# Kernel tuning notes

Hardware: AMD Instinct MI355X
Metric: run time of the kernel (lower is better)

Reference implementation:

```python
import jax, jax.numpy as jnp
import numpy as np
import math

HEADS = 16
HIDDEN = 1024
HEAD_DIM = HIDDEN // HEADS


def _split_heads(t):
    # (B, S, H*D) -> (B, H, S, D)
    b, s, _ = t.shape
    return t.reshape(b, s, HEADS, HEAD_DIM).transpose(0, 2, 1, 3)


def _rel_shift(x):
    # Transformer-XL relative shift: pad a zero column, reshape, drop first row.
    b, h, q, L = x.shape
    zero_pad = jnp.zeros((b, h, q, 1), dtype=x.dtype)
    x_padded = jnp.concatenate([zero_pad, x], axis=-1).reshape(b, h, L + 1, q)
    return x_padded[:, :, 1:, :].reshape(b, h, q, L)


def setup_inputs() -> dict:
    key = jax.random.key(0)
    ks = jax.random.split(key, 12)
    B, S, MEM = 4, 1024, 1024
    KV = S + MEM
    inp = {
        "x": jax.random.normal(ks[0], (B, S, HIDDEN), jnp.float32),
        "u": jax.random.normal(ks[1], (HEADS, HEAD_DIM), jnp.float32),
        "v_rel": jax.random.normal(ks[2], (HEADS, HEAD_DIM), jnp.float32),
        "rel": jax.random.normal(ks[3], (1, KV, HIDDEN), jnp.float32),
        "mask": jnp.zeros((1, 1, S, KV), jnp.int32),
        "past_key_values": jax.random.normal(ks[4], (B, MEM, HIDDEN), jnp.float32),
        "Wq": jax.random.normal(ks[5], (HIDDEN, HIDDEN), jnp.float32) * 0.02,
        "Wk": jax.random.normal(ks[6], (HIDDEN, HIDDEN), jnp.float32) * 0.02,
        "Wv": jax.random.normal(ks[7], (HIDDEN, HIDDEN), jnp.float32) * 0.02,
        "Wr": jax.random.normal(ks[8], (HIDDEN, HIDDEN), jnp.float32) * 0.02,
        "Wfc": jax.random.normal(ks[9], (HIDDEN, HIDDEN), jnp.float32) * 0.02,
        "bfc": jnp.zeros((HIDDEN,), jnp.float32),
    }
    return inp


def reference(x, u, v_rel, rel, mask, past_key_values, Wq, Wk, Wv, Wr, Wfc, bfc):
    # Transformer-XL style relative-position multi-head attention (eval mode, dropout off).
    x_extra = jnp.concatenate([past_key_values, x], axis=1)  # (B, KV, H*D)
    q = _split_heads(x @ Wq.T)          # (B, H, S, D)
    k = _split_heads(x_extra @ Wk.T)    # (B, H, KV, D)
    v = _split_heads(x_extra @ Wv.T)    # (B, H, KV, D)
    # rel: (1, KV, HIDDEN) -> r: (1, H, KV, D)
    r = (rel @ Wr.T).reshape(1, rel.shape[1], HEADS, HEAD_DIM).transpose(0, 2, 1, 3)

    term_AC = jnp.einsum("bhsd,bhkd->bhsk", q + u[None, :, None, :], k)
    term_BD = jnp.einsum("bhsd,xhkd->bhsk", q + v_rel[None, :, None, :], r)
    term_BD = _rel_shift(term_BD)

    attn = (term_AC + term_BD) / math.sqrt(HEAD_DIM)
    attn = jnp.where(mask == 1, -jnp.inf, attn)
    attn = jax.nn.softmax(attn, axis=-1)
    attn = jnp.where(jnp.isnan(attn), 0.0, attn)  # nan-cleanup from fully-masked rows

    out = jnp.einsum("bhsk,bhkd->bhsd", attn, v)
    out = out.transpose(0, 2, 1, 3).reshape(x.shape[0], x.shape[1], HIDDEN)
    out = out @ Wfc.T + bfc + x
    return out
```

## Files before the change

kernel.cpp:

```cpp
#include <hip/hip_runtime.h>
#include <stdint.h>


typedef unsigned short u16;
typedef __bf16 v8bf __attribute__((ext_vector_type(8)));
typedef float v4f __attribute__((ext_vector_type(4)));
typedef short v4s __attribute__((ext_vector_type(4)));

__device__ __forceinline__ v4f mfma16(v8bf a, v8bf b, v4f c) {
  return __builtin_amdgcn_mfma_f32_16x16x32_bf16(a, b, c, 0, 0, 0);
}

__device__ __forceinline__ u16 f2bf(float f) {
  uint32_t u = __builtin_bit_cast(uint32_t, f);
  return (u16)((u + 0x7fffu + ((u >> 16) & 1u)) >> 16);
}

__device__ __forceinline__ void async16(const u16* g, u16* l) {
  __builtin_amdgcn_global_load_lds(
      (const __attribute__((address_space(1))) void*)g,
      (__attribute__((address_space(3))) void*)l, 16, 0, 0);
}

__device__ __forceinline__ float bperm(int idx, float v) {
  return __builtin_bit_cast(
      float, __builtin_amdgcn_ds_bpermute(idx, __builtin_bit_cast(int, v)));
}

#if defined(__has_builtin)
#if __has_builtin(__builtin_amdgcn_ds_read_tr16_b64)
#define HAS_TR16 1
#endif
#endif

__device__ __forceinline__ v8bf vfrag(const u16* p) {
  v4s lo, hi;
#ifdef HAS_TR16
  lo = __builtin_amdgcn_ds_read_tr16_b64(
      (__attribute__((address_space(3))) v4s*)p);
  hi = __builtin_amdgcn_ds_read_tr16_b64(
      (__attribute__((address_space(3))) v4s*)(p + 256));
#else
#pragma unroll
  for (int j = 0; j < 4; ++j) {
    lo[j] = (short)p[j * 16];
    hi[j] = (short)p[256 + j * 16];
  }
#endif
  return __builtin_bit_cast(v8bf,
                            __builtin_shufflevector(lo, hi, 0, 1, 2, 3, 4, 5, 6, 7));
}

__global__ void conv_all_k(const float* __restrict__ past, const float* __restrict__ x,
                           const float* __restrict__ rel, const float* __restrict__ Wq,
                           const float* __restrict__ Wk, const float* __restrict__ Wv,
                           const float* __restrict__ Wr, const float* __restrict__ Wfc,
                           u16* __restrict__ xe, u16* __restrict__ xb,
                           u16* __restrict__ relb, u16* __restrict__ wdst,
                           u16* __restrict__ zrow) {
  int bid = blockIdx.x;
  if (bid < 8192) {
    int idx = bid * 256 + threadIdx.x;
    int e = idx << 2;
    int row = e >> 10, col = e & 1023;
    int b = row >> 11, t = row & 2047;
    const float* src = (t < 1024) ? past + ((((size_t)(b << 10)) + t) << 10) + col
                                  : x + ((((size_t)(b << 10)) + (t - 1024)) << 10) + col;
    float4 v = *(const float4*)src;
    ushort4 o = make_ushort4(f2bf(v.x), f2bf(v.y), f2bf(v.z), f2bf(v.w));
    *(ushort4*)(xe + e) = o;
    if (t >= 1024) {
      size_t xbi = ((((size_t)(b << 10)) + (t - 1024)) << 10) + col;
      *(ushort4*)(xb + xbi) = o;
    }
  } else if (bid < 10240) {
    int e = ((bid - 8192) * 256 + threadIdx.x) << 2;
    float4 v = *(const float4*)(rel + e);
    *(ushort4*)(relb + e) =
        make_ushort4(f2bf(v.x), f2bf(v.y), f2bf(v.z), f2bf(v.w));
  } else if (bid < 15360) {
    int wb = bid - 10240;
    int wsel = wb >> 10;
    const float* src = (wsel == 0) ? Wq
                     : (wsel == 1) ? Wk
                     : (wsel == 2) ? Wv
                     : (wsel == 3) ? Wr : Wfc;
    int e = ((wb & 1023) * 256 + threadIdx.x) << 2;
    float4 v = *(const float4*)(src + e);
    *(ushort4*)(wdst + (((size_t)wsel) << 20) + e) =
        make_ushort4(f2bf(v.x), f2bf(v.y), f2bf(v.z), f2bf(v.w));
  } else {
    *(ushort4*)(zrow + threadIdx.x * 4) = make_ushort4(0, 0, 0, 0);
  }
}

__device__ __forceinline__ void gemm_body(const u16* A, const u16* Bw, u16* o0, u16* o1,
                                          bool dual, const float* bias0, const float* bias1,
                                          int row0, int col0, u16* lA, u16* lB) {
  int t = threadIdx.x;
  int w = t >> 6, lane = t & 63, q = lane >> 4, l = lane & 15;
  int wy = w >> 1, wx = w & 1;
  v4f acc[4][4];
#pragma unroll
  for (int i = 0; i < 4; i++)
#pragma unroll
    for (int j = 0; j < 4; j++) acc[i][j] = v4f{0.f, 0.f, 0.f, 0.f};

  for (int kb = 0; kb < 1024; kb += 32) {
    __syncthreads();
#pragma unroll
    for (int p = 0; p < 2; ++p) {
      int g = (p << 8) + (w << 6) + lane;
      int m = g >> 2, cp = g & 3;
      int c = cp ^ ((m >> 1) & 3);
      async16(A + (((size_t)(row0 + m)) << 10) + kb + (c << 3),
              lA + ((p << 8) + (w << 6)) * 8);
      async16(Bw + (((size_t)(col0 + m)) << 10) + kb + (c << 3),
              lB + ((p << 8) + (w << 6)) * 8);
    }
    __syncthreads();
    v8bf af[4], bfr[4];
#pragma unroll
    for (int mt = 0; mt < 4; ++mt) {
      int ml = (wy << 6) + (mt << 4) + l;
      af[mt] = *(const v8bf*)&lA[(ml << 5) + ((q ^ ((ml >> 1) & 3)) << 3)];
      int nl = (wx << 6) + (mt << 4) + l;
      bfr[mt] = *(const v8bf*)&lB[(nl << 5) + ((q ^ ((nl >> 1) & 3)) << 3)];
    }
#pragma unroll
    for (int mt = 0; mt < 4; ++mt)
#pragma unroll
      for (int nt = 0; nt < 4; ++nt)
        acc[mt][nt] = mfma16(af[mt], bfr[nt], acc[mt][nt]);
  }

  float b0[4], b1[4];
  if (dual) {
#pragma unroll
    for (int nt = 0; nt < 4; ++nt) {
      int gcol = col0 + (wx << 6) + (nt << 4) + l;
      b0[nt] = bias0[gcol];
      b1[nt] = bias1[gcol];
    }
  }
#pragma unroll
  for (int mt = 0; mt < 4; ++mt)
#pragma unroll
    for (int nt = 0; nt < 4; ++nt)
#pragma unroll
      for (int rr = 0; rr < 4; ++rr) {
        int grow = row0 + (wy << 6) + (mt << 4) + (q << 2) + rr;
        int gcol = col0 + (wx << 6) + (nt << 4) + l;
        size_t idx = (((size_t)grow) << 10) + gcol;
        float v = acc[mt][nt][rr];
        if (dual) {
          o0[idx] = f2bf(v + b0[nt]);
          o1[idx] = f2bf(v + b1[nt]);
        } else {
          o0[idx] = f2bf(v);
        }
      }
}

__launch_bounds__(256)
__global__ void gemm_qkvr(const u16* __restrict__ xb, const u16* __restrict__ xe,
                          const u16* __restrict__ relb, const u16* __restrict__ wqb,
                          const u16* __restrict__ wkb, const u16* __restrict__ wvb,
                          const u16* __restrict__ wrb, u16* __restrict__ Qu,
                          u16* __restrict__ Qv, u16* __restrict__ Kbf,
                          u16* __restrict__ Vbf, u16* __restrict__ Rpb,
                          const float* __restrict__ u, const float* __restrict__ vr) {
  __shared__ __align__(16) u16 lA[128 * 32];
  __shared__ __align__(16) u16 lB[128 * 32];
  int y = blockIdx.y;
  const u16 *A, *Bw;
  u16 *o0, *o1 = nullptr;
  bool dual = false;
  int row0;
  if (y < 32) {
    A = xb; Bw = wqb; o0 = Qu; o1 = Qv; dual = true; row0 = y << 7;
  } else if (y < 96) {
    A = xe; Bw = wkb; o0 = Kbf; row0 = (y - 32) << 7;
  } else if (y < 160) {
    A = xe; Bw = wvb; o0 = Vbf; row0 = (y - 96) << 7;
  } else {
    A = relb; Bw = wrb; o0 = Rpb; row0 = (y - 160) << 7;
  }
  gemm_body(A, Bw, o0, o1, dual, u, vr, row0, blockIdx.x << 7, lA, lB);
}

__launch_bounds__(256)
__global__ void gemm_fin(const u16* __restrict__ A, const u16* __restrict__ Bw,
                         float* __restrict__ of, const float* __restrict__ bias0,
                         const float* __restrict__ resid) {
  __shared__ __align__(16) u16 lA[128 * 32];
  __shared__ __align__(16) u16 lB[128 * 32];
  int t = threadIdx.x;
  int w = t >> 6, lane = t & 63, q = lane >> 4, l = lane & 15;
  int wy = w >> 1, wx = w & 1;
  int row0 = blockIdx.y << 7, col0 = blockIdx.x << 7;
  v4f acc[4][4];
#pragma unroll
  for (int i = 0; i < 4; i++)
#pragma unroll
    for (int j = 0; j < 4; j++) acc[i][j] = v4f{0.f, 0.f, 0.f, 0.f};

  for (int kb = 0; kb < 1024; kb += 32) {
    __syncthreads();
#pragma unroll
    for (int p = 0; p < 2; ++p) {
      int g = (p << 8) + (w << 6) + lane;
      int m = g >> 2, cp = g & 3;
      int c = cp ^ ((m >> 1) & 3);
      async16(A + (((size_t)(row0 + m)) << 10) + kb + (c << 3),
              lA + ((p << 8) + (w << 6)) * 8);
      async16(Bw + (((size_t)(col0 + m)) << 10) + kb + (c << 3),
              lB + ((p << 8) + (w << 6)) * 8);
    }
    __syncthreads();
    v8bf af[4], bfr[4];
#pragma unroll
    for (int mt = 0; mt < 4; ++mt) {
      int ml = (wy << 6) + (mt << 4) + l;
      af[mt] = *(const v8bf*)&lA[(ml << 5) + ((q ^ ((ml >> 1) & 3)) << 3)];
      int nl = (wx << 6) + (mt << 4) + l;
      bfr[mt] = *(const v8bf*)&lB[(nl << 5) + ((q ^ ((nl >> 1) & 3)) << 3)];
    }
#pragma unroll
    for (int mt = 0; mt < 4; ++mt)
#pragma unroll
      for (int nt = 0; nt < 4; ++nt)
        acc[mt][nt] = mfma16(af[mt], bfr[nt], acc[mt][nt]);
  }

  float b0[4];
#pragma unroll
  for (int nt = 0; nt < 4; ++nt) b0[nt] = bias0[col0 + (wx << 6) + (nt << 4) + l];
#pragma unroll
  for (int mt = 0; mt < 4; ++mt)
#pragma unroll
    for (int nt = 0; nt < 4; ++nt)
#pragma unroll
      for (int rr = 0; rr < 4; ++rr) {
        int grow = row0 + (wy << 6) + (mt << 4) + (q << 2) + rr;
        int gcol = col0 + (wx << 6) + (nt << 4) + l;
        size_t idx = (((size_t)grow) << 10) + gcol;
        of[idx] = acc[mt][nt][rr] + b0[nt] + resid[idx];
      }
}

__launch_bounds__(256, 3)
__global__ void attn_k(const u16* __restrict__ Qu, const u16* __restrict__ Qv,
                       const u16* __restrict__ Kb, const u16* __restrict__ Vb,
                       const u16* __restrict__ Rp, u16* __restrict__ AO) {
  __shared__ __align__(16) u16 lK[64 * 64];
  __shared__ __align__(16) u16 lV[8 * 528];
  __shared__ __align__(16) u16 lR[192 * 64];
  __shared__ __align__(16) u16 lP[4][16 * 72];

  int t = threadIdx.x;
  int w = t >> 6, lane = t & 63, q = lane >> 4, l = lane & 15;
  int i0 = blockIdx.x << 6;
  int bh = blockIdx.y, b = bh >> 4, h = bh & 15;

  v8bf fqu[2], fqv[2], fqv1[2];
  {
    int m = i0 + (w << 4) + l;
    const u16* pu = Qu + ((((size_t)(b << 10)) + m) << 10) + (h << 6);
    fqu[0] = *(const v8bf*)(pu + q * 8);
    fqu[1] = *(const v8bf*)(pu + 32 + q * 8);
    const u16* pv = Qv + ((((size_t)(b << 10)) + m) << 10) + (h << 6);
    fqv[0] = *(const v8bf*)(pv + q * 8);
    fqv[1] = *(const v8bf*)(pv + 32 + q * 8);
    int m1 = min(m + 1, 1023);
    const u16* pv1 = Qv + ((((size_t)(b << 10)) + m1) << 10) + (h << 6);
    fqv1[0] = *(const v8bf*)(pv1 + q * 8);
    fqv1[1] = *(const v8bf*)(pv1 + 32 + q * 8);
  }

  v4f accO[4];
#pragma unroll
  for (int i = 0; i < 4; i++) accO[i] = v4f{0.f, 0.f, 0.f, 0.f};
  float psum[4] = {0.f, 0.f, 0.f, 0.f};
  const float SC = 0.125f * 1.44269504088896340736f;

  u16* Pw = &lP[w][0];
  const u16* vtb = lV + q * 528 + l;
  int rbase = 48 - (w << 4);

  int gidx[4];
  bool ghi[4];
#pragma unroll
  for (int rr = 0; rr < 4; ++rr) {
    int s = l + 15 - ((q << 2) + rr);
    gidx[rr] = ((q << 4) + (s & 15)) << 2;
    ghi[rr] = (s & 16) != 0;
  }

  int rb0 = 960 - i0;
  int r192 = rb0 % 192;

#pragma unroll
  for (int p = 0; p < 4; ++p) {
    int off = (p << 5) + (w << 3);
    int base = r192 + off;
    if (base >= 192) base -= 192;
    int rr = off + (lane >> 3);
    int c = (lane & 7) ^ (rr & 7);
    async16(Rp + (((size_t)(rb0 + rr)) << 10) + (h << 6) + (c << 3),
            lR + (base << 6));
  }

  for (int jt = 0; jt < 32; ++jt) {
    int j0 = jt << 6;

    __syncthreads();
#pragma unroll
    for (int p = 0; p < 2; ++p) {
      int g = (p << 8) + t;
      int kv = g >> 3, cp = g & 7, c = cp ^ (kv & 7);
      async16(Kb + ((((size_t)(b << 11)) + j0 + kv) << 10) + (h << 6) + (c << 3),
              lK + ((p << 8) + (w << 6)) * 8);
    }
#pragma unroll
    for (int p = 0; p < 2; ++p) {
      int s = (p << 8) + t;
      int kv = ((s >> 5) << 2) + ((s >> 1) & 3);
      int d = (((s >> 3) & 3) << 4) + ((s & 1) << 3);
      async16(Vb + ((((size_t)(b << 11)) + j0 + kv) << 10) + (h << 6) + d,
              lV + ((p << 2) + w) * 528);
    }
    if (jt < 31) {
      int sb = r192 + 128;
      if (sb >= 192) sb -= 192;
#pragma unroll
      for (int p = 0; p < 2; ++p) {
        int off = (p << 5) + (w << 3);
        int rr = off + (lane >> 3);
        int c = (lane & 7) ^ (rr & 7);
        int rowg = rb0 + 128 + rr;
        if (rowg >= 2049) rowg -= 2049;
        async16(Rp + (((size_t)rowg) << 10) + (h << 6) + (c << 3),
                lR + ((sb + off) << 6));
      }
    }
    __syncthreads();

    __builtin_amdgcn_s_setprio(1);
    v4f sc[4];
#pragma unroll
    for (int nt = 0; nt < 4; ++nt) {
      v4f a = v4f{0.f, 0.f, 0.f, 0.f};
      int row = (nt << 4) + l;
      a = mfma16(fqu[0], *(const v8bf*)&lK[((row << 3) + (q ^ (row & 7))) << 3], a);
      a = mfma16(fqu[1], *(const v8bf*)&lK[((row << 3) + ((4 + q) ^ (row & 7))) << 3], a);
      sc[nt] = a;
    }

    v4f eacc[5];
#pragma unroll
    for (int et = 0; et < 5; ++et) {
      int ps = r192 + rbase + (et << 4);
      if (ps >= 192) ps -= 192;
      int rrow = ps + l;
      v8bf r0 = *(const v8bf*)&lR[((rrow << 3) + (q ^ (rrow & 7))) << 3];
      v8bf r1 = *(const v8bf*)&lR[((rrow << 3) + ((4 + q) ^ (rrow & 7))) << 3];
      v4f a = v4f{0.f, 0.f, 0.f, 0.f};
      if (__builtin_amdgcn_readfirstlane(rb0 + rbase + (et << 4)) >= 2048) {
        a = mfma16(fqv1[0], r0, a);
        a = mfma16(fqv1[1], r1, a);
      } else {
        a = mfma16(fqv[0], r0, a);
        a = mfma16(fqv[1], r1, a);
      }
      eacc[et] = a;
    }
    __builtin_amdgcn_s_setprio(0);

#pragma unroll
    for (int rr = 0; rr < 4; ++rr) {
      float r0 = bperm(gidx[rr], eacc[0][rr]);
      float r1 = bperm(gidx[rr], eacc[1][rr]);
      float r2 = bperm(gidx[rr], eacc[2][rr]);
      float r3 = bperm(gidx[rr], eacc[3][rr]);
      float r4 = bperm(gidx[rr], eacc[4][rr]);
      sc[0][rr] += ghi[rr] ? r1 : r0;
      sc[1][rr] += ghi[rr] ? r2 : r1;
      sc[2][rr] += ghi[rr] ? r3 : r2;
      sc[3][rr] += ghi[rr] ? r4 : r3;
    }

#pragma unroll
    for (int nt = 0; nt < 4; ++nt)
#pragma unroll
      for (int rr = 0; rr < 4; ++rr) {
        float pv = __builtin_amdgcn_exp2f(sc[nt][rr] * SC);
        psum[rr] += pv;
        Pw[((q << 2) + rr) * 72 + (nt << 4) + l] = __builtin_bit_cast(u16, (__bf16)pv);
      }

    v8bf fp0 = *(const v8bf*)&Pw[l * 72 + (q << 3)];
    v8bf fp1 = *(const v8bf*)&Pw[l * 72 + 32 + (q << 3)];
    __builtin_amdgcn_s_setprio(1);
#pragma unroll
    for (int nt = 0; nt < 4; ++nt) {
      accO[nt] = mfma16(fp0, vfrag(vtb + (nt << 6)), accO[nt]);
      accO[nt] = mfma16(fp1, vfrag(vtb + (nt << 6) + 2112), accO[nt]);
    }
    __builtin_amdgcn_s_setprio(0);

    rb0 += 64;
    r192 += 64;
    if (r192 >= 192) r192 -= 192;
  }

#pragma unroll
  for (int rr = 0; rr < 4; ++rr) {
    float v = psum[rr];
    v += __shfl_xor(v, 1);
    v += __shfl_xor(v, 2);
    v += __shfl_xor(v, 4);
    v += __shfl_xor(v, 8);
    psum[rr] = 1.0f / v;
  }
#pragma unroll
  for (int nt = 0; nt < 4; ++nt)
#pragma unroll
    for (int rr = 0; rr < 4; ++rr) {
      int i = i0 + (w << 4) + (q << 2) + rr;
      int col = (h << 6) + (nt << 4) + l;
      AO[((((size_t)(b << 10)) + i) << 10) + col] = f2bf(accO[nt][rr] * psum[rr]);
    }
}


extern "C" void kernel_launch(void* const* d_in, const int* in_sizes, int n_in,
                              void* d_out, int out_size, void* d_ws, size_t ws_size,
                              hipStream_t stream) {
  const float* x    = (const float*)d_in[0];
  const float* u    = (const float*)d_in[1];
  const float* vr   = (const float*)d_in[2];
  const float* rel  = (const float*)d_in[3];
  const float* past = (const float*)d_in[5];
  const float* Wq   = (const float*)d_in[6];
  const float* Wk   = (const float*)d_in[7];
  const float* Wv   = (const float*)d_in[8];
  const float* Wr   = (const float*)d_in[9];
  const float* Wfc  = (const float*)d_in[10];
  const float* bfc  = (const float*)d_in[11];
  float* out = (float*)d_out;

  char* ws = (char*)d_ws;
  u16* xe   = (u16*)(ws + 0);
  u16* xb   = (u16*)(ws + 16777216);
  u16* relb = (u16*)(ws + 25165824);
  u16* wqb  = (u16*)(ws + 29360128);
  u16* wkb  = (u16*)(ws + 31457280);
  u16* wvb  = (u16*)(ws + 33554432);
  u16* wrb  = (u16*)(ws + 35651584);
  u16* wfcb = (u16*)(ws + 37748736);
  u16* Qu   = (u16*)(ws + 39845888);
  u16* Qv   = (u16*)(ws + 48234496);
  u16* Kbf  = (u16*)(ws + 56623104);
  u16* Vbf  = (u16*)(ws + 73400320);
  u16* Rpb  = (u16*)(ws + 90177536);
  u16* AOb  = (u16*)(ws + 94373888);
  if (ws_size < 102762496ull) return;

  conv_all_k<<<dim3(15361), dim3(256), 0, stream>>>(
      past, x, rel, Wq, Wk, Wv, Wr, Wfc, xe, xb, relb, wqb, Rpb + 2048 * 1024);

  gemm_qkvr<<<dim3(8, 176), dim3(256), 0, stream>>>(
      xb, xe, relb, wqb, wkb, wvb, wrb, Qu, Qv, Kbf, Vbf, Rpb, u, vr);

  attn_k<<<dim3(16, 64), dim3(256), 0, stream>>>(Qu, Qv, Kbf, Vbf, Rpb, AOb);

  gemm_fin<<<dim3(8, 32), dim3(256), 0, stream>>>(AOb, wfcb, out, bfc, x);
}
```

Before: 386.2 us.

## Double attention query tile to 128 rows with 8 waves sharing K/V/R tiles

Each attention block now covers 128 query rows with 512 threads (8 waves), so each K, V and R tile loaded into LDS is reused by twice as many waves and global traffic per query row halves. The R ring buffer grows to 256 rows with power-of-two masking in place of the modulo-192 bookkeeping. The trailing __syncthreads is replaced by explicit vmcnt waits plus s_barrier. The grid shrinks to 512 blocks, which reduces parallelism, and the larger LDS footprint may limit occupancy.

```diff
diff --git a/kernel.cpp b/kernel.cpp
--- a/kernel.cpp
+++ b/kernel.cpp
@@ -249,18 +249,18 @@
       }
 }
 
-__launch_bounds__(256, 3)
+__launch_bounds__(512, 4)
 __global__ void attn_k(const u16* __restrict__ Qu, const u16* __restrict__ Qv,
                        const u16* __restrict__ Kb, const u16* __restrict__ Vb,
                        const u16* __restrict__ Rp, u16* __restrict__ AO) {
   __shared__ __align__(16) u16 lK[64 * 64];
   __shared__ __align__(16) u16 lV[8 * 528];
-  __shared__ __align__(16) u16 lR[192 * 64];
-  __shared__ __align__(16) u16 lP[4][16 * 72];
+  __shared__ __align__(16) u16 lR[256 * 64];
+  __shared__ __align__(16) u16 lP[8][16 * 72];
 
   int t = threadIdx.x;
   int w = t >> 6, lane = t & 63, q = lane >> 4, l = lane & 15;
-  int i0 = blockIdx.x << 6;
+  int i0 = blockIdx.x << 7;
   int bh = blockIdx.y, b = bh >> 4, h = bh & 15;
 
   v8bf fqu[2], fqv[2], fqv1[2];
@@ -286,7 +286,7 @@
 
   u16* Pw = &lP[w][0];
   const u16* vtb = lV + q * 528 + l;
-  int rbase = 48 - (w << 4);
+  int rbase = 112 - (w << 4);
 
   int gidx[4];
   bool ghi[4];
@@ -297,54 +297,48 @@
     ghi[rr] = (s & 16) != 0;
   }
 
-  int rb0 = 960 - i0;
-  int r192 = rb0 % 192;
-
-#pragma unroll
-  for (int p = 0; p < 4; ++p) {
-    int off = (p << 5) + (w << 3);
-    int base = r192 + off;
-    if (base >= 192) base -= 192;
-    int rr = off + (lane >> 3);
+  int rb0 = 896 - i0;
+
+#pragma unroll
+  for (int p = 0; p < 3; ++p) {
+    int rr = (p << 6) + (t >> 3);
     int c = (lane & 7) ^ (rr & 7);
+    int sb = ((rb0 + (p << 6)) & 255) + (w << 3);
     async16(Rp + (((size_t)(rb0 + rr)) << 10) + (h << 6) + (c << 3),
-            lR + (base << 6));
+            lR + (sb << 6));
   }
 
   for (int jt = 0; jt < 32; ++jt) {
     int j0 = jt << 6;
 
     __syncthreads();
-#pragma unroll
-    for (int p = 0; p < 2; ++p) {
-      int g = (p << 8) + t;
-      int kv = g >> 3, cp = g & 7, c = cp ^ (kv & 7);
+
+    {
+      int kv = t >> 3, cp = t & 7, c = cp ^ (kv & 7);
       async16(Kb + ((((size_t)(b << 11)) + j0 + kv) << 10) + (h << 6) + (c << 3),
-              lK + ((p << 8) + (w << 6)) * 8);
-    }
-#pragma unroll
-    for (int p = 0; p < 2; ++p) {
-      int s = (p << 8) + t;
-      int kv = ((s >> 5) << 2) + ((s >> 1) & 3);
-      int d = (((s >> 3) & 3) << 4) + ((s & 1) << 3);
+              lK + (w << 6) * 8);
+    }
+    {
+      int kv = ((t >> 5) << 2) + ((t >> 1) & 3);
+      int d = (((t >> 3) & 3) << 4) + ((t & 1) << 3);
       async16(Vb + ((((size_t)(b << 11)) + j0 + kv) << 10) + (h << 6) + d,
-              lV + ((p << 2) + w) * 528);
+              lV + w * 528);
     }
     if (jt < 31) {
-      int sb = r192 + 128;
-      if (sb >= 192) sb -= 192;
-#pragma unroll
-      for (int p = 0; p < 2; ++p) {
-        int off = (p << 5) + (w << 3);
-        int rr = off + (lane >> 3);
-        int c = (lane & 7) ^ (rr & 7);
-        int rowg = rb0 + 128 + rr;
-        if (rowg >= 2049) rowg -= 2049;
-        async16(Rp + (((size_t)rowg) << 10) + (h << 6) + (c << 3),
-                lR + ((sb + off) << 6));
-      }
-    }
-    __syncthreads();
+      int rr = t >> 3;
+      int c = (lane & 7) ^ (rr & 7);
+      int rowg = rb0 + 192 + rr;
+      if (rowg >= 2049) rowg -= 2049;
+      int sb = ((rb0 + 192) & 255) + (w << 3);
+      async16(Rp + (((size_t)rowg) << 10) + (h << 6) + (c << 3),
+              lR + (sb << 6));
+      asm volatile("s_waitcnt vmcnt(1)" ::: "memory");
+    } else {
+      asm volatile("s_waitcnt vmcnt(0)" ::: "memory");
+    }
+    __builtin_amdgcn_s_barrier();
+    asm volatile("" ::: "memory");
+    __builtin_amdgcn_sched_barrier(0);
 
     __builtin_amdgcn_s_setprio(1);
     v4f sc[4];
@@ -360,8 +354,7 @@
     v4f eacc[5];
 #pragma unroll
     for (int et = 0; et < 5; ++et) {
-      int ps = r192 + rbase + (et << 4);
-      if (ps >= 192) ps -= 192;
+      int ps = ((rb0 & 255) + rbase + (et << 4)) & 255;
       int rrow = ps + l;
       v8bf r0 = *(const v8bf*)&lR[((rrow << 3) + (q ^ (rrow & 7))) << 3];
       v8bf r1 = *(const v8bf*)&lR[((rrow << 3) + ((4 + q) ^ (rrow & 7))) << 3];
@@ -410,8 +403,6 @@
     __builtin_amdgcn_s_setprio(0);
 
     rb0 += 64;
-    r192 += 64;
-    if (r192 >= 192) r192 -= 192;
   }
 
 #pragma unroll
@@ -473,7 +464,7 @@
   gemm_qkvr<<<dim3(8, 176), dim3(256), 0, stream>>>(
       xb, xe, relb, wqb, wkb, wvb, wrb, Qu, Qv, Kbf, Vbf, Rpb, u, vr);
 
-  attn_k<<<dim3(16, 64), dim3(256), 0, stream>>>(Qu, Qv, Kbf, Vbf, Rpb, AOb);
+  attn_k<<<dim3(8, 64), dim3(512), 0, stream>>>(Qu, Qv, Kbf, Vbf, Rpb, AOb);
 
   gemm_fin<<<dim3(8, 32), dim3(256), 0, stream>>>(AOb, wfcb, out, bfc, x);
 }
```

After: 347.0 us. 1.11x faster.
